# Optimization experiments

Measured on AMD Instinct MI355X. Metric: run time of the kernel, lower is better.

## Reference

```python
import jax, jax.numpy as jnp
import numpy as np

BATCH, DIM, ORDER = 16384, 1024, 3

def setup_inputs() -> dict:
    key = jax.random.key(0)
    k1, k2, k3 = jax.random.split(key, 3)
    x0 = jax.random.normal(k1, (BATCH, DIM), dtype=jnp.float32)
    # xavier-uniform init scale for w of shape (d, 1): sqrt(6/(d+1))
    limit = float(np.sqrt(6.0 / (DIM + 1)))
    W = jax.random.uniform(k2, (ORDER, DIM), dtype=jnp.float32, minval=-limit, maxval=limit)
    B = jnp.zeros((ORDER, DIM), dtype=jnp.float32)
    return {"x0": x0, "W": W, "B": B}

def reference(x0, W, B):
    # CrossLayer: xi_next = (x0 xi^T) w + b + xi == x0 * (xi . w) + b + xi
    # (outer product followed by matmul with w collapses to a dot-product scale)
    xi = x0
    for l in range(W.shape[0]):  # small fixed number of cross layers
        s = xi @ W[l]                      # [B]  dot(xi, w_l)
        xi = x0 * s[:, None] + B[l] + xi   # [B, D]
    return xi
```

## Files before the change

### kernel.cpp

```cpp
#include <hip/hip_runtime.h>


#define CN_BATCH 16384
#define CN_DIM   1024

#define WAVES_PER_BLOCK 4
#define ROWS_PER_WAVE   2
#define ROWS_PER_BLOCK  (WAVES_PER_BLOCK * ROWS_PER_WAVE)
#define GRID_BLOCKS     (CN_BATCH / ROWS_PER_BLOCK)

typedef float f32x4 __attribute__((ext_vector_type(4)));

__device__ __forceinline__ float fma4(f32x4 x, f32x4 w, float acc) {
    acc = fmaf(x.x, w.x, acc); acc = fmaf(x.y, w.y, acc);
    acc = fmaf(x.z, w.z, acc); acc = fmaf(x.w, w.w, acc);
    return acc;
}

__global__ __launch_bounds__(256, 4) void
crossnet_kernel(const float* __restrict__ x0,
                const float* __restrict__ W,
                const float* __restrict__ B,
                float* __restrict__ out)
{
    const int tid  = threadIdx.x;
    const int wave = tid >> 6;
    const int lane = tid & 63;
    const int off0 = lane * 4;

    const size_t row0 = ((size_t)blockIdx.x * WAVES_PER_BLOCK + wave) * ROWS_PER_WAVE;
    const float* __restrict__ xr = x0 + row0 * CN_DIM;

    f32x4 xv[ROWS_PER_WAVE][4];
#pragma unroll
    for (int r = 0; r < ROWS_PER_WAVE; ++r)
#pragma unroll
        for (int c = 0; c < 4; ++c)
            xv[r][c] = *reinterpret_cast<const f32x4*>(xr + r * CN_DIM + c * 256 + off0);

    f32x4 w0[4], w1[4], w2[4], bs[4];
    float t1 = 0.f, t2 = 0.f;
#pragma unroll
    for (int c = 0; c < 4; ++c) {
        const int off = c * 256 + off0;
        w0[c] = *reinterpret_cast<const f32x4*>(W + 0 * CN_DIM + off);
        w1[c] = *reinterpret_cast<const f32x4*>(W + 1 * CN_DIM + off);
        w2[c] = *reinterpret_cast<const f32x4*>(W + 2 * CN_DIM + off);
        const f32x4 b0 = *reinterpret_cast<const f32x4*>(B + 0 * CN_DIM + off);
        const f32x4 b1 = *reinterpret_cast<const f32x4*>(B + 1 * CN_DIM + off);
        const f32x4 b2 = *reinterpret_cast<const f32x4*>(B + 2 * CN_DIM + off);
        bs[c] = b0 + b1 + b2;
        t1 = fma4(b0, w1[c], t1);
        t2 = fma4(b0 + b1, w2[c], t2);
    }

    float a[ROWS_PER_WAVE][3];
#pragma unroll
    for (int r = 0; r < ROWS_PER_WAVE; ++r) {
        a[r][0] = 0.f; a[r][1] = 0.f; a[r][2] = 0.f;
    }
#pragma unroll
    for (int c = 0; c < 4; ++c) {
#pragma unroll
        for (int r = 0; r < ROWS_PER_WAVE; ++r) {
            a[r][0] = fma4(xv[r][c], w0[c], a[r][0]);
            a[r][1] = fma4(xv[r][c], w1[c], a[r][1]);
            a[r][2] = fma4(xv[r][c], w2[c], a[r][2]);
        }
    }

#pragma unroll
    for (int o = 1; o < 64; o <<= 1) {
#pragma unroll
        for (int r = 0; r < ROWS_PER_WAVE; ++r) {
            a[r][0] += __shfl_xor(a[r][0], o, 64);
            a[r][1] += __shfl_xor(a[r][1], o, 64);
            a[r][2] += __shfl_xor(a[r][2], o, 64);
        }
        t1 += __shfl_xor(t1, o, 64);
        t2 += __shfl_xor(t2, o, 64);
    }

#pragma unroll
    for (int r = 0; r < ROWS_PER_WAVE; ++r) {
        const float s0 = a[r][0];
        const float s1 = fmaf(1.f + s0, a[r][1], t1);
        const float s2 = fmaf(1.f + s0 + s1, a[r][2], t2);
        const float cf = 1.f + s0 + s1 + s2;
        float* __restrict__ orow = out + (row0 + r) * CN_DIM;
#pragma unroll
        for (int c = 0; c < 4; ++c) {
            f32x4 o;
            o.x = fmaf(xv[r][c].x, cf, bs[c].x);
            o.y = fmaf(xv[r][c].y, cf, bs[c].y);
            o.z = fmaf(xv[r][c].z, cf, bs[c].z);
            o.w = fmaf(xv[r][c].w, cf, bs[c].w);
            *reinterpret_cast<f32x4*>(orow + c * 256 + off0) = o;
        }
    }
}

extern "C" void kernel_launch(void* const* d_in, const int* in_sizes, int n_in,
                              void* d_out, int out_size, void* d_ws, size_t ws_size,
                              hipStream_t stream)
{
    const float* x0 = (const float*)d_in[0];
    const float* W  = (const float*)d_in[1];
    const float* B  = (const float*)d_in[2];
    float* out      = (float*)d_out;

    dim3 grid(GRID_BLOCKS);
    dim3 block(WAVES_PER_BLOCK * 64);
    crossnet_kernel<<<grid, block, 0, stream>>>(x0, W, B, out);
}
```

Baseline: 117.9 us.

## Software-pipeline row groups per wave with register double-buffered prefetch

Each wave now handles eight rows in four groups of two, loading the next group's x0 rows into registers while computing and storing the current group. W/B loads and bias dot products are amortized over more rows, and launch bounds are relaxed to allow more registers. The grid shrinks fourfold, reducing the number of resident waves available to hide memory latency.

Result: no change. 116.2 us (-1.5%).

```diff
diff --git a/kernel.cpp b/kernel.cpp
--- a/kernel.cpp
+++ b/kernel.cpp
@@ -5,7 +5,9 @@
 #define CN_DIM   1024
 
 #define WAVES_PER_BLOCK 4
-#define ROWS_PER_WAVE   2
+#define GROUPS          4
+#define GROUP_ROWS      2
+#define ROWS_PER_WAVE   (GROUPS * GROUP_ROWS)
 #define ROWS_PER_BLOCK  (WAVES_PER_BLOCK * ROWS_PER_WAVE)
 #define GRID_BLOCKS     (CN_BATCH / ROWS_PER_BLOCK)
 
@@ -17,7 +19,7 @@
     return acc;
 }
 
-__global__ __launch_bounds__(256, 4) void
+__global__ __launch_bounds__(256, 2) void
 crossnet_kernel(const float* __restrict__ x0,
                 const float* __restrict__ W,
                 const float* __restrict__ B,
@@ -31,12 +33,12 @@
     const size_t row0 = ((size_t)blockIdx.x * WAVES_PER_BLOCK + wave) * ROWS_PER_WAVE;
     const float* __restrict__ xr = x0 + row0 * CN_DIM;
 
-    f32x4 xv[ROWS_PER_WAVE][4];
+    f32x4 cur[GROUP_ROWS][4], nxt[GROUP_ROWS][4];
 #pragma unroll
-    for (int r = 0; r < ROWS_PER_WAVE; ++r)
+    for (int r = 0; r < GROUP_ROWS; ++r)
 #pragma unroll
         for (int c = 0; c < 4; ++c)
-            xv[r][c] = *reinterpret_cast<const f32x4*>(xr + r * CN_DIM + c * 256 + off0);
+            cur[r][c] = *reinterpret_cast<const f32x4*>(xr + r * CN_DIM + c * 256 + off0);
 
     f32x4 w0[4], w1[4], w2[4], bs[4];
     float t1 = 0.f, t2 = 0.f;
@@ -54,49 +56,69 @@
         t2 = fma4(b0 + b1, w2[c], t2);
     }
 
-    float a[ROWS_PER_WAVE][3];
 #pragma unroll
-    for (int r = 0; r < ROWS_PER_WAVE; ++r) {
-        a[r][0] = 0.f; a[r][1] = 0.f; a[r][2] = 0.f;
-    }
+    for (int g = 0; g < GROUPS; ++g) {
+        if (g + 1 < GROUPS) {
 #pragma unroll
-    for (int c = 0; c < 4; ++c) {
+            for (int r = 0; r < GROUP_ROWS; ++r)
 #pragma unroll
-        for (int r = 0; r < ROWS_PER_WAVE; ++r) {
-            a[r][0] = fma4(xv[r][c], w0[c], a[r][0]);
-            a[r][1] = fma4(xv[r][c], w1[c], a[r][1]);
-            a[r][2] = fma4(xv[r][c], w2[c], a[r][2]);
+                for (int c = 0; c < 4; ++c)
+                    nxt[r][c] = *reinterpret_cast<const f32x4*>(
+                        xr + (size_t)((g + 1) * GROUP_ROWS + r) * CN_DIM + c * 256 + off0);
         }
-    }
+
+        float a[GROUP_ROWS][3];
+#pragma unroll
+        for (int r = 0; r < GROUP_ROWS; ++r) {
+            a[r][0] = 0.f; a[r][1] = 0.f; a[r][2] = 0.f;
+        }
+#pragma unroll
+        for (int c = 0; c < 4; ++c) {
+#pragma unroll
+            for (int r = 0; r < GROUP_ROWS; ++r) {
+                a[r][0] = fma4(cur[r][c], w0[c], a[r][0]);
+                a[r][1] = fma4(cur[r][c], w1[c], a[r][1]);
+                a[r][2] = fma4(cur[r][c], w2[c], a[r][2]);
+            }
+        }
 
 #pragma unroll
-    for (int o = 1; o < 64; o <<= 1) {
+        for (int o = 1; o < 64; o <<= 1) {
 #pragma unroll
-        for (int r = 0; r < ROWS_PER_WAVE; ++r) {
-            a[r][0] += __shfl_xor(a[r][0], o, 64);
-            a[r][1] += __shfl_xor(a[r][1], o, 64);
-            a[r][2] += __shfl_xor(a[r][2], o, 64);
+            for (int r = 0; r < GROUP_ROWS; ++r) {
+                a[r][0] += __shfl_xor(a[r][0], o, 64);
+                a[r][1] += __shfl_xor(a[r][1], o, 64);
+                a[r][2] += __shfl_xor(a[r][2], o, 64);
+            }
+            if (g == 0) {
+                t1 += __shfl_xor(t1, o, 64);
+                t2 += __shfl_xor(t2, o, 64);
+            }
         }
-        t1 += __shfl_xor(t1, o, 64);
-        t2 += __shfl_xor(t2, o, 64);
-    }
 
 #pragma unroll
-    for (int r = 0; r < ROWS_PER_WAVE; ++r) {
-        const float s0 = a[r][0];
-        const float s1 = fmaf(1.f + s0, a[r][1], t1);
-        const float s2 = fmaf(1.f + s0 + s1, a[r][2], t2);
-        const float cf = 1.f + s0 + s1 + s2;
-        float* __restrict__ orow = out + (row0 + r) * CN_DIM;
+        for (int r = 0; r < GROUP_ROWS; ++r) {
+            const float s0 = a[r][0];
+            const float s1 = fmaf(1.f + s0, a[r][1], t1);
+            const float s2 = fmaf(1.f + s0 + s1, a[r][2], t2);
+            const float cf = 1.f + s0 + s1 + s2;
+            float* __restrict__ orow = out + (row0 + (size_t)(g * GROUP_ROWS + r)) * CN_DIM;
 #pragma unroll
-        for (int c = 0; c < 4; ++c) {
-            f32x4 o;
-            o.x = fmaf(xv[r][c].x, cf, bs[c].x);
-            o.y = fmaf(xv[r][c].y, cf, bs[c].y);
-            o.z = fmaf(xv[r][c].z, cf, bs[c].z);
-            o.w = fmaf(xv[r][c].w, cf, bs[c].w);
-            *reinterpret_cast<f32x4*>(orow + c * 256 + off0) = o;
+            for (int c = 0; c < 4; ++c) {
+                f32x4 o;
+                o.x = fmaf(cur[r][c].x, cf, bs[c].x);
+                o.y = fmaf(cur[r][c].y, cf, bs[c].y);
+                o.z = fmaf(cur[r][c].z, cf, bs[c].z);
+                o.w = fmaf(cur[r][c].w, cf, bs[c].w);
+                *reinterpret_cast<f32x4*>(orow + c * 256 + off0) = o;
+            }
         }
+
+#pragma unroll
+        for (int r = 0; r < GROUP_ROWS; ++r)
+#pragma unroll
+            for (int c = 0; c < 4; ++c)
+                cur[r][c] = nxt[r][c];
     }
 }
 
```

## Software-pipeline row loads and use DPP wave reductions with more rows per wave

Applied to the files above, without the earlier changes.

Each wave now handles four rows instead of two, streaming one row at a time: the next row is prefetched while the current row's dot products, reduction and output store run. The cross-lane reduction switches from xor-shuffles (ds_bpermute) to DPP row_shr/row_bcast adds plus a readlane of lane 63, which should be cheaper per step. The goal is to overlap memory latency and amortize the per-wave W/B setup, at the cost of halving the grid, which may reduce parallelism and memory-level concurrency on a bandwidth-bound kernel.

After: 119.8 us. About the same (+1.7%).

```diff
diff --git a/kernel.cpp b/kernel.cpp
--- a/kernel.cpp
+++ b/kernel.cpp
@@ -5,7 +5,7 @@
 #define CN_DIM   1024
 
 #define WAVES_PER_BLOCK 4
-#define ROWS_PER_WAVE   2
+#define ROWS_PER_WAVE   4
 #define ROWS_PER_BLOCK  (WAVES_PER_BLOCK * ROWS_PER_WAVE)
 #define GRID_BLOCKS     (CN_BATCH / ROWS_PER_BLOCK)
 
@@ -15,6 +15,24 @@
     acc = fmaf(x.x, w.x, acc); acc = fmaf(x.y, w.y, acc);
     acc = fmaf(x.z, w.z, acc); acc = fmaf(x.w, w.w, acc);
     return acc;
+}
+
+#define DPP_ADD(x, ctrl, rmask)                                            \
+    ((x) + __int_as_float(__builtin_amdgcn_update_dpp(                     \
+         0, __float_as_int(x), (ctrl), (rmask), 0xf, false)))
+
+__device__ __forceinline__ float wave_sum63(float x) {
+    x = DPP_ADD(x, 0x111, 0xf);
+    x = DPP_ADD(x, 0x112, 0xf);
+    x = DPP_ADD(x, 0x114, 0xf);
+    x = DPP_ADD(x, 0x118, 0xf);
+    x = DPP_ADD(x, 0x142, 0xa);
+    x = DPP_ADD(x, 0x143, 0xc);
+    return x;
+}
+
+__device__ __forceinline__ float bcast63(float x) {
+    return __int_as_float(__builtin_amdgcn_readlane(__float_as_int(x), 63));
 }
 
 __global__ __launch_bounds__(256, 4) void
@@ -31,12 +49,10 @@
     const size_t row0 = ((size_t)blockIdx.x * WAVES_PER_BLOCK + wave) * ROWS_PER_WAVE;
     const float* __restrict__ xr = x0 + row0 * CN_DIM;
 
-    f32x4 xv[ROWS_PER_WAVE][4];
+    f32x4 cur[4], nxt[4];
 #pragma unroll
-    for (int r = 0; r < ROWS_PER_WAVE; ++r)
-#pragma unroll
-        for (int c = 0; c < 4; ++c)
-            xv[r][c] = *reinterpret_cast<const f32x4*>(xr + r * CN_DIM + c * 256 + off0);
+    for (int c = 0; c < 4; ++c)
+        cur[c] = *reinterpret_cast<const f32x4*>(xr + c * 256 + off0);
 
     f32x4 w0[4], w1[4], w2[4], bs[4];
     float t1 = 0.f, t2 = 0.f;
@@ -53,50 +69,50 @@
         t1 = fma4(b0, w1[c], t1);
         t2 = fma4(b0 + b1, w2[c], t2);
     }
-
-    float a[ROWS_PER_WAVE][3];
-#pragma unroll
-    for (int r = 0; r < ROWS_PER_WAVE; ++r) {
-        a[r][0] = 0.f; a[r][1] = 0.f; a[r][2] = 0.f;
-    }
-#pragma unroll
-    for (int c = 0; c < 4; ++c) {
-#pragma unroll
-        for (int r = 0; r < ROWS_PER_WAVE; ++r) {
-            a[r][0] = fma4(xv[r][c], w0[c], a[r][0]);
-            a[r][1] = fma4(xv[r][c], w1[c], a[r][1]);
-            a[r][2] = fma4(xv[r][c], w2[c], a[r][2]);
-        }
-    }
-
-#pragma unroll
-    for (int o = 1; o < 64; o <<= 1) {
-#pragma unroll
-        for (int r = 0; r < ROWS_PER_WAVE; ++r) {
-            a[r][0] += __shfl_xor(a[r][0], o, 64);
-            a[r][1] += __shfl_xor(a[r][1], o, 64);
-            a[r][2] += __shfl_xor(a[r][2], o, 64);
-        }
-        t1 += __shfl_xor(t1, o, 64);
-        t2 += __shfl_xor(t2, o, 64);
-    }
+    const float t1s = bcast63(wave_sum63(t1));
+    const float t2s = bcast63(wave_sum63(t2));
 
 #pragma unroll
     for (int r = 0; r < ROWS_PER_WAVE; ++r) {
-        const float s0 = a[r][0];
-        const float s1 = fmaf(1.f + s0, a[r][1], t1);
-        const float s2 = fmaf(1.f + s0 + s1, a[r][2], t2);
+        if (r + 1 < ROWS_PER_WAVE) {
+#pragma unroll
+            for (int c = 0; c < 4; ++c)
+                nxt[c] = *reinterpret_cast<const f32x4*>(
+                    xr + (size_t)(r + 1) * CN_DIM + c * 256 + off0);
+        }
+
+        float a0 = 0.f, a1 = 0.f, a2 = 0.f;
+#pragma unroll
+        for (int c = 0; c < 4; ++c) {
+            a0 = fma4(cur[c], w0[c], a0);
+            a1 = fma4(cur[c], w1[c], a1);
+            a2 = fma4(cur[c], w2[c], a2);
+        }
+
+        a0 = wave_sum63(a0);
+        a1 = wave_sum63(a1);
+        a2 = wave_sum63(a2);
+        const float s0 = bcast63(a0);
+        const float A1 = bcast63(a1);
+        const float A2 = bcast63(a2);
+
+        const float s1 = fmaf(1.f + s0, A1, t1s);
+        const float s2 = fmaf(1.f + s0 + s1, A2, t2s);
         const float cf = 1.f + s0 + s1 + s2;
-        float* __restrict__ orow = out + (row0 + r) * CN_DIM;
+
+        float* __restrict__ orow = out + (row0 + (size_t)r) * CN_DIM;
 #pragma unroll
         for (int c = 0; c < 4; ++c) {
             f32x4 o;
-            o.x = fmaf(xv[r][c].x, cf, bs[c].x);
-            o.y = fmaf(xv[r][c].y, cf, bs[c].y);
-            o.z = fmaf(xv[r][c].z, cf, bs[c].z);
-            o.w = fmaf(xv[r][c].w, cf, bs[c].w);
+            o.x = fmaf(cur[c].x, cf, bs[c].x);
+            o.y = fmaf(cur[c].y, cf, bs[c].y);
+            o.z = fmaf(cur[c].z, cf, bs[c].z);
+            o.w = fmaf(cur[c].w, cf, bs[c].w);
             *reinterpret_cast<f32x4*>(orow + c * 256 + off0) = o;
         }
+
+#pragma unroll
+        for (int c = 0; c < 4; ++c) cur[c] = nxt[c];
     }
 }
 
```

## Software-pipeline rows per wave with triple-buffered register loads

Applied to the files above, without the earlier changes.

Each wave now processes 8 rows instead of 2, using a three-slot register ring. While the dot products of the current row are computed, the previous row's output is stored and a row two ahead is prefetched. This is meant to overlap global load latency with compute and the shuffle reductions, and to amortize the W/B loads and bias dot products over more rows. In exchange the grid has a quarter as many blocks and the occupancy hint drops to 2 blocks per CU, so less parallelism is available to hide latency.

Result: no change. 116.5 us (-1.2%).

```diff
diff --git a/kernel.cpp b/kernel.cpp
--- a/kernel.cpp
+++ b/kernel.cpp
@@ -5,7 +5,7 @@
 #define CN_DIM   1024
 
 #define WAVES_PER_BLOCK 4
-#define ROWS_PER_WAVE   2
+#define ROWS_PER_WAVE   8
 #define ROWS_PER_BLOCK  (WAVES_PER_BLOCK * ROWS_PER_WAVE)
 #define GRID_BLOCKS     (CN_BATCH / ROWS_PER_BLOCK)
 
@@ -17,7 +17,7 @@
     return acc;
 }
 
-__global__ __launch_bounds__(256, 4) void
+__global__ __launch_bounds__(256, 2) void
 crossnet_kernel(const float* __restrict__ x0,
                 const float* __restrict__ W,
                 const float* __restrict__ B,
@@ -31,12 +31,12 @@
     const size_t row0 = ((size_t)blockIdx.x * WAVES_PER_BLOCK + wave) * ROWS_PER_WAVE;
     const float* __restrict__ xr = x0 + row0 * CN_DIM;
 
-    f32x4 xv[ROWS_PER_WAVE][4];
+    f32x4 xb[3][4];
 #pragma unroll
-    for (int r = 0; r < ROWS_PER_WAVE; ++r)
+    for (int r = 0; r < 3; ++r)
 #pragma unroll
         for (int c = 0; c < 4; ++c)
-            xv[r][c] = *reinterpret_cast<const f32x4*>(xr + r * CN_DIM + c * 256 + off0);
+            xb[r][c] = *reinterpret_cast<const f32x4*>(xr + r * CN_DIM + c * 256 + off0);
 
     f32x4 w0[4], w1[4], w2[4], bs[4];
     float t1 = 0.f, t2 = 0.f;
@@ -54,47 +54,81 @@
         t2 = fma4(b0 + b1, w2[c], t2);
     }
 
-    float a[ROWS_PER_WAVE][3];
+    float a0 = 0.f, a1 = 0.f, a2 = 0.f;
 #pragma unroll
-    for (int r = 0; r < ROWS_PER_WAVE; ++r) {
-        a[r][0] = 0.f; a[r][1] = 0.f; a[r][2] = 0.f;
+    for (int c = 0; c < 4; ++c) {
+        a0 = fma4(xb[0][c], w0[c], a0);
+        a1 = fma4(xb[0][c], w1[c], a1);
+        a2 = fma4(xb[0][c], w2[c], a2);
     }
 #pragma unroll
-    for (int c = 0; c < 4; ++c) {
-#pragma unroll
-        for (int r = 0; r < ROWS_PER_WAVE; ++r) {
-            a[r][0] = fma4(xv[r][c], w0[c], a[r][0]);
-            a[r][1] = fma4(xv[r][c], w1[c], a[r][1]);
-            a[r][2] = fma4(xv[r][c], w2[c], a[r][2]);
-        }
-    }
-
-#pragma unroll
     for (int o = 1; o < 64; o <<= 1) {
-#pragma unroll
-        for (int r = 0; r < ROWS_PER_WAVE; ++r) {
-            a[r][0] += __shfl_xor(a[r][0], o, 64);
-            a[r][1] += __shfl_xor(a[r][1], o, 64);
-            a[r][2] += __shfl_xor(a[r][2], o, 64);
-        }
+        a0 += __shfl_xor(a0, o, 64);
+        a1 += __shfl_xor(a1, o, 64);
+        a2 += __shfl_xor(a2, o, 64);
         t1 += __shfl_xor(t1, o, 64);
         t2 += __shfl_xor(t2, o, 64);
     }
+    float s0 = a0;
+    float s1 = fmaf(1.f + s0, a1, t1);
+    float s2 = fmaf(1.f + s0 + s1, a2, t2);
+    float cf_prev = 1.f + s0 + s1 + s2;
 
 #pragma unroll
-    for (int r = 0; r < ROWS_PER_WAVE; ++r) {
-        const float s0 = a[r][0];
-        const float s1 = fmaf(1.f + s0, a[r][1], t1);
-        const float s2 = fmaf(1.f + s0 + s1, a[r][2], t2);
-        const float cf = 1.f + s0 + s1 + s2;
-        float* __restrict__ orow = out + (row0 + r) * CN_DIM;
+    for (int r = 1; r < ROWS_PER_WAVE; ++r) {
+        const int cbuf = r % 3;
+        const int sbuf = (r - 1) % 3;
+
+        a0 = 0.f; a1 = 0.f; a2 = 0.f;
+#pragma unroll
+        for (int c = 0; c < 4; ++c) {
+            a0 = fma4(xb[cbuf][c], w0[c], a0);
+            a1 = fma4(xb[cbuf][c], w1[c], a1);
+            a2 = fma4(xb[cbuf][c], w2[c], a2);
+        }
+
+        {
+            float* __restrict__ orow = out + (row0 + (size_t)(r - 1)) * CN_DIM;
+#pragma unroll
+            for (int c = 0; c < 4; ++c) {
+                f32x4 o;
+                o.x = fmaf(xb[sbuf][c].x, cf_prev, bs[c].x);
+                o.y = fmaf(xb[sbuf][c].y, cf_prev, bs[c].y);
+                o.z = fmaf(xb[sbuf][c].z, cf_prev, bs[c].z);
+                o.w = fmaf(xb[sbuf][c].w, cf_prev, bs[c].w);
+                *reinterpret_cast<f32x4*>(orow + c * 256 + off0) = o;
+            }
+        }
+
+        if (r + 2 < ROWS_PER_WAVE) {
+#pragma unroll
+            for (int c = 0; c < 4; ++c)
+                xb[sbuf][c] = *reinterpret_cast<const f32x4*>(
+                    xr + (size_t)(r + 2) * CN_DIM + c * 256 + off0);
+        }
+
+#pragma unroll
+        for (int o = 1; o < 64; o <<= 1) {
+            a0 += __shfl_xor(a0, o, 64);
+            a1 += __shfl_xor(a1, o, 64);
+            a2 += __shfl_xor(a2, o, 64);
+        }
+        s0 = a0;
+        s1 = fmaf(1.f + s0, a1, t1);
+        s2 = fmaf(1.f + s0 + s1, a2, t2);
+        cf_prev = 1.f + s0 + s1 + s2;
+    }
+
+    {
+        const int sbuf = (ROWS_PER_WAVE - 1) % 3;
+        float* __restrict__ orow = out + (row0 + (size_t)(ROWS_PER_WAVE - 1)) * CN_DIM;
 #pragma unroll
         for (int c = 0; c < 4; ++c) {
             f32x4 o;
-            o.x = fmaf(xv[r][c].x, cf, bs[c].x);
-            o.y = fmaf(xv[r][c].y, cf, bs[c].y);
-            o.z = fmaf(xv[r][c].z, cf, bs[c].z);
-            o.w = fmaf(xv[r][c].w, cf, bs[c].w);
+            o.x = fmaf(xb[sbuf][c].x, cf_prev, bs[c].x);
+            o.y = fmaf(xb[sbuf][c].y, cf_prev, bs[c].y);
+            o.z = fmaf(xb[sbuf][c].z, cf_prev, bs[c].z);
+            o.w = fmaf(xb[sbuf][c].w, cf_prev, bs[c].w);
             *reinterpret_cast<f32x4*>(orow + c * 256 + off0) = o;
         }
     }
```
